# Optimization experiments

Hardware: AMD Instinct MI355X
Metric: run time of the kernel (lower is better)

Reference implementation:

```python
import jax, jax.numpy as jnp
import numpy as np
from jax import lax

EMBED = 512
HEADS = 8
KD = EMBED // HEADS  # key_dim == head_dim (value_factor=1)


def setup_inputs() -> dict:
    key = jax.random.key(0)
    ks = jax.random.split(key, 13)
    b, h, w = 4, 128, 128
    s = 0.02
    return {
        "x": jax.random.normal(ks[0], (b, h, w, EMBED), jnp.float32),
        "mask_h": jax.random.normal(ks[1], (HEADS, h, h), jnp.float32),
        "mask_w": jax.random.normal(ks[2], (HEADS, w, w), jnp.float32),
        "Wq": jax.random.normal(ks[3], (EMBED, EMBED), jnp.float32) * s,
        "bq": jnp.zeros((EMBED,), jnp.float32),
        "Wk": jax.random.normal(ks[4], (EMBED, EMBED), jnp.float32) * s,
        "bk": jnp.zeros((EMBED,), jnp.float32),
        "Wv": jax.random.normal(ks[5], (EMBED, EMBED), jnp.float32) * s,
        "bv": jnp.zeros((EMBED,), jnp.float32),
        "lepe_w": jax.random.normal(ks[6], (5, 5, 1, EMBED), jnp.float32) * s,  # depthwise 5x5, HWIO
        "lepe_b": jnp.zeros((EMBED,), jnp.float32),
        "Wo": jax.random.normal(ks[7], (EMBED, EMBED), jnp.float32) * s,
        "bo": jnp.zeros((EMBED,), jnp.float32),
    }


def reference(x, mask_h, mask_w, Wq, bq, Wk, bk, Wv, bv, lepe_w, lepe_b, Wo, bo):
    b, h, w, _ = x.shape
    scaling = KD ** -0.5
    q = x @ Wq + bq                      # (b,h,w,C)
    k = (x @ Wk + bk) * scaling
    v = x @ Wv + bv

    # depthwise-conv positional term (LePE), 5x5 pad 2, groups=C
    lepe = lax.conv_general_dilated(
        v, lepe_w, window_strides=(1, 1), padding=[(2, 2), (2, 2)],
        dimension_numbers=("NHWC", "HWIO", "NHWC"), feature_group_count=EMBED,
    ) + lepe_b

    qr = q.reshape(b, h, w, HEADS, KD)
    kr = k.reshape(b, h, w, HEADS, KD)
    vr = v.reshape(b, h, w, HEADS, KD)

    # width-axis attention (per row), additive per-head decay mask
    sw = jnp.einsum("bhqnd,bhknd->bhnqk", qr, kr) + mask_w[None, None]  # (b,h,n,w,w)
    Aw = jax.nn.softmax(sw, axis=-1)
    o1 = jnp.einsum("bhnqk,bhknd->bhqnd", Aw, vr)                       # (b,h,w,n,d)

    # height-axis attention (per column) on the width-pass output
    sh = jnp.einsum("bqwnd,bkwnd->bwnqk", qr, kr) + mask_h[None, None]  # (b,w,n,h,h)
    Ah = jax.nn.softmax(sh, axis=-1)
    o2 = jnp.einsum("bwnqk,bkwnd->bqwnd", Ah, o1)                       # (b,h,w,n,d)

    out = o2.reshape(b, h, w, EMBED) + lepe
    return out @ Wo + bo
```

## Files before the change

kernel.cpp:

```cpp
#include <hip/hip_runtime.h>
#include <stdint.h>
#include <stddef.h>

typedef unsigned short u16;
typedef __attribute__((ext_vector_type(8))) short bf16x8;
typedef __attribute__((ext_vector_type(4))) float f32x4;

__device__ __forceinline__ u16 f2bf(float f) {
  union { float f; uint32_t u; } v; v.f = f;
  uint32_t u = v.u;
  return (u16)((u + 0x7FFFu + ((u >> 16) & 1u)) >> 16);
}
__device__ __forceinline__ float bf2f(u16 b) {
  union { uint32_t u; float f; } v; v.u = ((uint32_t)b) << 16;
  return v.f;
}

__device__ __forceinline__ void glds16(const u16* g, u16* l) {
  __builtin_amdgcn_global_load_lds((const __attribute__((address_space(1))) void*)g,
                                   (__attribute__((address_space(3))) void*)l, 16, 0, 0);
}

#define MFMA(a, b, c) __builtin_amdgcn_mfma_f32_16x16x32_bf16((a), (b), (c), 0, 0, 0)


__global__ __launch_bounds__(256) void k_cvt_bf16(const float* __restrict__ in,
                                                  u16* __restrict__ out, int n) {
  int i = (blockIdx.x * 256 + threadIdx.x) * 8;
  if (i >= n) return;
  const float4* p = (const float4*)(in + i);
  float4 a = p[0], b = p[1];
  union { bf16x8 v; u16 s[8]; } o;
  o.s[0] = f2bf(a.x); o.s[1] = f2bf(a.y); o.s[2] = f2bf(a.z); o.s[3] = f2bf(a.w);
  o.s[4] = f2bf(b.x); o.s[5] = f2bf(b.y); o.s[6] = f2bf(b.z); o.s[7] = f2bf(b.w);
  *(bf16x8*)(out + i) = o.v;
}

__global__ __launch_bounds__(256) void k_build_wqkv(
    const float* __restrict__ Wq, const float* __restrict__ bq,
    const float* __restrict__ Wk, const float* __restrict__ bk,
    const float* __restrict__ Wv, const float* __restrict__ bv,
    u16* __restrict__ wT, float* __restrict__ bias) {
  int idx = blockIdx.x * 256 + threadIdx.x;
  int n = idx >> 9, k = idx & 511;
  const float* W; const float* B; int nn; float s = 1.0f;
  if (n < 512)       { W = Wq; B = bq; nn = n; }
  else if (n < 1024) { W = Wk; B = bk; nn = n - 512; s = 0.125f; }
  else               { W = Wv; B = bv; nn = n - 1024; }
  wT[idx] = f2bf(W[(size_t)k * 512 + nn] * s);
  if (k == 0) bias[n] = B[nn] * s;
}

__global__ __launch_bounds__(256) void k_build_wo(const float* __restrict__ Wo,
                                                  u16* __restrict__ wT) {
  int idx = blockIdx.x * 256 + threadIdx.x;
  int n = idx >> 9, k = idx & 511;
  wT[idx] = f2bf(Wo[(size_t)k * 512 + n]);
}


__device__ __forceinline__ void stageH(const u16* __restrict__ src, int ld, size_t grow0,
                                       int kt, int row0, u16* lmat, int t) {
  #pragma unroll
  for (int it = 0; it < 2; ++it) {
    int e = it * 4096 + t * 8;
    int row = row0 + (e >> 6);
    int ch = (e >> 3) & 7;
    int cs = ch ^ (row & 7);
    glds16(src + (grow0 + row) * (size_t)ld + kt * 64 + cs * 8, lmat + row * 64 + ch * 8);
  }
}

__device__ __forceinline__ bf16x8 ldfrag(const u16* lmat, int row, int c) {
  return *(const bf16x8*)(lmat + row * 64 + ((c ^ (row & 7)) << 3));
}

template<bool STAGE, bool VM8>
__device__ __forceinline__ void process_tile(
    const u16* __restrict__ A, int lda, size_t rowA0,
    const u16* __restrict__ BT, int ldb, size_t rowB0,
    u16* LAc, u16* LBc, int nxt,
    int wm, int wn, int fq, int fr, int t,
    f32x4 (&acc)[2][4][2][2])
{
  bf16x8 bA[4][2], bB[2][2][2];
  #pragma unroll
  for (int n = 0; n < 2; ++n)
    #pragma unroll
    for (int kk = 0; kk < 2; ++kk)
      bB[0][n][kk] = ldfrag(LBc, wn * 32 + n * 16 + fr, kk * 4 + fq);
  #pragma unroll
  for (int m = 0; m < 4; ++m)
    #pragma unroll
    for (int kk = 0; kk < 2; ++kk)
      bA[m][kk] = ldfrag(LAc, wm * 64 + m * 16 + fr, kk * 4 + fq);
  __builtin_amdgcn_s_setprio(1);
  #pragma unroll
  for (int m = 0; m < 4; ++m)
    #pragma unroll
    for (int n = 0; n < 2; ++n)
      #pragma unroll
      for (int kk = 0; kk < 2; ++kk)
        acc[0][m][0][n] = MFMA(bA[m][kk], bB[0][n][kk], acc[0][m][0][n]);
  __builtin_amdgcn_s_setprio(0);
  __builtin_amdgcn_s_barrier();
  #pragma unroll
  for (int n = 0; n < 2; ++n)
    #pragma unroll
    for (int kk = 0; kk < 2; ++kk)
      bB[1][n][kk] = ldfrag(LBc, 128 + wn * 32 + n * 16 + fr, kk * 4 + fq);
  if (STAGE) {
    stageH(A, lda, rowA0, nxt, 0, LAc, t);
    stageH(BT, ldb, rowB0, nxt, 0, LBc, t);
  }
  __builtin_amdgcn_s_setprio(1);
  #pragma unroll
  for (int m = 0; m < 4; ++m)
    #pragma unroll
    for (int n = 0; n < 2; ++n)
      #pragma unroll
      for (int kk = 0; kk < 2; ++kk)
        acc[0][m][1][n] = MFMA(bA[m][kk], bB[1][n][kk], acc[0][m][1][n]);
  __builtin_amdgcn_s_setprio(0);
  __builtin_amdgcn_s_barrier();
  #pragma unroll
  for (int m = 0; m < 4; ++m)
    #pragma unroll
    for (int kk = 0; kk < 2; ++kk)
      bA[m][kk] = ldfrag(LAc, 128 + wm * 64 + m * 16 + fr, kk * 4 + fq);
  if (STAGE) stageH(BT, ldb, rowB0, nxt, 128, LBc, t);
  __builtin_amdgcn_s_setprio(1);
  #pragma unroll
  for (int m = 0; m < 4; ++m)
    #pragma unroll
    for (int n = 0; n < 2; ++n)
      #pragma unroll
      for (int kk = 0; kk < 2; ++kk)
        acc[1][m][0][n] = MFMA(bA[m][kk], bB[0][n][kk], acc[1][m][0][n]);
  __builtin_amdgcn_s_setprio(0);
  __builtin_amdgcn_s_barrier();
  if (STAGE) stageH(A, lda, rowA0, nxt, 128, LAc, t);
  __builtin_amdgcn_s_setprio(1);
  #pragma unroll
  for (int m = 0; m < 4; ++m)
    #pragma unroll
    for (int n = 0; n < 2; ++n)
      #pragma unroll
      for (int kk = 0; kk < 2; ++kk)
        acc[1][m][1][n] = MFMA(bA[m][kk], bB[1][n][kk], acc[1][m][1][n]);
  __builtin_amdgcn_s_setprio(0);
  if (VM8) asm volatile("s_waitcnt vmcnt(8)" ::: "memory");
  else     asm volatile("s_waitcnt vmcnt(0)" ::: "memory");
  __builtin_amdgcn_s_barrier();
}

template<bool OUT_F32, int NTN>
__global__ __launch_bounds__(512, 2) void k_gemm256(
    const u16* __restrict__ A, int lda,
    const u16* __restrict__ BT, int ldb,
    const float* __restrict__ bias,
    void* __restrict__ Cp, int ldc)
{
  __shared__ u16 lds[65536];
  u16* LA0 = lds;
  u16* LB0 = lds + 16384;
  u16* LA1 = lds + 32768;
  u16* LB1 = lds + 49152;

  const int t = threadIdx.x, l = t & 63, w = t >> 6;
  const int wm = w >> 2, wn = w & 3;
  const int fq = l >> 4, fr = l & 15;

  const int bid = blockIdx.x;
  const int cpx = gridDim.x >> 3;
  const int swz = (bid & 7) * cpx + (bid >> 3);
  const int tn = swz % NTN, tm = swz / NTN;
  const size_t rowA0 = (size_t)tm * 256;
  const size_t rowB0 = (size_t)tn * 256;

  f32x4 acc[2][4][2][2];
  #pragma unroll
  for (int a = 0; a < 2; ++a)
    #pragma unroll
    for (int m = 0; m < 4; ++m)
      #pragma unroll
      for (int b = 0; b < 2; ++b)
        #pragma unroll
        for (int n = 0; n < 2; ++n) acc[a][m][b][n] = (f32x4){0.f, 0.f, 0.f, 0.f};

  stageH(A,  lda, rowA0, 0, 0,   LA0, t); stageH(A,  lda, rowA0, 0, 128, LA0, t);
  stageH(BT, ldb, rowB0, 0, 0,   LB0, t); stageH(BT, ldb, rowB0, 0, 128, LB0, t);
  stageH(A,  lda, rowA0, 1, 0,   LA1, t); stageH(A,  lda, rowA0, 1, 128, LA1, t);
  stageH(BT, ldb, rowB0, 1, 0,   LB1, t); stageH(BT, ldb, rowB0, 1, 128, LB1, t);
  asm volatile("s_waitcnt vmcnt(8)" ::: "memory");
  __builtin_amdgcn_s_barrier();

  for (int i = 0; i < 3; ++i) {
    process_tile<true, true>(A, lda, rowA0, BT, ldb, rowB0, LA0, LB0, 2 * i + 2,
                             wm, wn, fq, fr, t, acc);
    process_tile<true, true>(A, lda, rowA0, BT, ldb, rowB0, LA1, LB1, 2 * i + 3,
                             wm, wn, fq, fr, t, acc);
  }
  process_tile<false, false>(A, lda, rowA0, BT, ldb, rowB0, LA0, LB0, 0,
                             wm, wn, fq, fr, t, acc);
  process_tile<false, false>(A, lda, rowA0, BT, ldb, rowB0, LA1, LB1, 0,
                             wm, wn, fq, fr, t, acc);

  #pragma unroll
  for (int nh = 0; nh < 2; ++nh)
    #pragma unroll
    for (int n = 0; n < 2; ++n) {
      int col = (int)rowB0 + nh * 128 + wn * 32 + n * 16 + fr;
      float bb = bias[col];
      #pragma unroll
      for (int mh = 0; mh < 2; ++mh)
        #pragma unroll
        for (int m = 0; m < 4; ++m) {
          #pragma unroll
          for (int r = 0; r < 4; ++r) {
            size_t row = rowA0 + mh * 128 + wm * 64 + m * 16 + fq * 4 + r;
            float v = acc[mh][m][nh][n][r] + bb;
            if (OUT_F32) ((float*)Cp)[row * ldc + col] = v;
            else         ((u16*)Cp)[row * ldc + col] = f2bf(v);
          }
        }
    }
}


__global__ __launch_bounds__(256) void k_lepe(
    const u16* __restrict__ qkv, const float* __restrict__ w5,
    const float* __restrict__ lb, u16* __restrict__ outp)
{
  __shared__ u16 wlds[12800];
  #pragma unroll
  for (int j = 0; j < 50; ++j) {
    int idx = j * 256 + threadIdx.x;
    wlds[idx] = f2bf(w5[idx]);
  }
  __syncthreads();

  const int t = threadIdx.x, w = t >> 6, l = t & 63;
  const int c0 = l << 3;
  const int bid = blockIdx.x;
  const int x = (bid & 31) * 4 + w;
  const int y0 = ((bid >> 5) & 15) * 8;
  const int b = bid >> 9;

  float acc[8][8];
  {
    float4 b0 = *(const float4*)(lb + c0);
    float4 b1 = *(const float4*)(lb + c0 + 4);
    #pragma unroll
    for (int tt = 0; tt < 8; ++tt) {
      acc[tt][0] = b0.x; acc[tt][1] = b0.y; acc[tt][2] = b0.z; acc[tt][3] = b0.w;
      acc[tt][4] = b1.x; acc[tt][5] = b1.y; acc[tt][6] = b1.z; acc[tt][7] = b1.w;
    }
  }

  #pragma unroll
  for (int r = 0; r < 12; ++r) {
    int yy = y0 + r - 2;
    if ((unsigned)yy < 128u) {
      #pragma unroll
      for (int dx = 0; dx < 5; ++dx) {
        int xx = x + dx - 2;
        if ((unsigned)xx < 128u) {
          union { bf16x8 v; u16 s[8]; } v8;
          v8.v = *(const bf16x8*)(qkv + (size_t)((b * 128 + yy) * 128 + xx) * 1536
                                  + 1024 + c0);
          float vf[8];
          #pragma unroll
          for (int j = 0; j < 8; ++j) vf[j] = bf2f(v8.s[j]);
          #pragma unroll
          for (int tt = 0; tt < 8; ++tt) {
            int dy = r - tt;
            if (dy >= 0 && dy <= 4) {
              union { bf16x8 v; u16 s[8]; } w8;
              w8.v = *(const bf16x8*)(wlds + (dy * 5 + dx) * 512 + c0);
              #pragma unroll
              for (int j = 0; j < 8; ++j)
                acc[tt][j] += vf[j] * bf2f(w8.s[j]);
            }
          }
        }
      }
    }
  }

  #pragma unroll
  for (int tt = 0; tt < 8; ++tt) {
    size_t tok = (size_t)(b * 128 + y0 + tt) * 128 + x;
    union { bf16x8 v; u16 s[8]; } ov;
    #pragma unroll
    for (int j = 0; j < 8; ++j) ov.s[j] = f2bf(acc[tt][j]);
    *(bf16x8*)(outp + tok * 512 + c0) = ov.v;
  }
}


template<int AXIS>
__global__ __launch_bounds__(512) void k_attn(
    const u16* qkv, const float* __restrict__ mask,
    const u16* __restrict__ lepe, u16* outp)
{
  __shared__ u16 smem[24576];
  u16* q_s = smem;
  u16* k_s = smem + 8192;
  u16* vT  = smem + 16384;
  u16* P   = smem;

  const int t = threadIdx.x, w = t >> 6, l = t & 63;
  const int fq = l >> 4, fr = l & 15;
  const int line = blockIdx.x, head = blockIdx.y, b = blockIdx.z;
  const int coff = head * 64;
  const size_t base0 = (AXIS == 0) ? ((size_t)(b * 128 + line) * 128)
                                   : ((size_t)b * 16384 + line);
  const size_t tstr = (AXIS == 0) ? 1 : 128;

  #pragma unroll
  for (int it = 0; it < 2; ++it) {
    int ee = it * 4096 + t * 8;
    int row = ee >> 6;
    int cs = ((ee >> 3) & 7) ^ (row & 7);
    size_t tok = base0 + (size_t)row * tstr;
    glds16(qkv + tok * 1536 +       coff + cs * 8, q_s + it * 4096 + w * 512);
    glds16(qkv + tok * 1536 + 512 + coff + cs * 8, k_s + it * 4096 + w * 512);
  }
  {
    int chunk = t & 7, kgrp = t >> 3;
    #pragma unroll
    for (int p = 0; p < 2; ++p) {
      int kidx = p * 64 + kgrp;
      size_t tok = base0 + (size_t)kidx * tstr;
      union { bf16x8 v; u16 s[8]; } v8;
      v8.v = *(const bf16x8*)(qkv + tok * 1536 + 1024 + coff + chunk * 8);
      #pragma unroll
      for (int j = 0; j < 8; ++j) {
        int d = chunk * 8 + j;
        int byt = d * 256 + ((2 * kidx) ^ (j << 4) ^ (chunk << 5));
        *(u16*)((char*)vT + byt) = v8.s[j];
      }
    }
  }
  __syncthreads();

  f32x4 acc[8];
  #pragma unroll
  for (int n = 0; n < 8; ++n) acc[n] = (f32x4){0.f, 0.f, 0.f, 0.f};

  #pragma unroll
  for (int kk = 0; kk < 2; ++kk) {
    int arow = w * 16 + fr;
    int ac = (kk * 4 + fq) ^ (arow & 7);
    bf16x8 af = *(const bf16x8*)(q_s + arow * 64 + ac * 8);
    #pragma unroll
    for (int n = 0; n < 8; ++n) {
      int brow = n * 16 + fr;
      int bc = (kk * 4 + fq) ^ (brow & 7);
      bf16x8 bfr = *(const bf16x8*)(k_s + brow * 64 + bc * 8);
      acc[n] = MFMA(af, bfr, acc[n]);
    }
  }

  const float* mbase = mask + (size_t)head * 16384;
  const int q0 = w * 16 + fq * 4;
  #pragma unroll
  for (int n = 0; n < 8; ++n) {
    const float* mp = mbase + (size_t)q0 * 128 + n * 16 + fr;
    #pragma unroll
    for (int r = 0; r < 4; ++r) acc[n][r] += mp[(size_t)r * 128];
  }
  #pragma unroll
  for (int r = 0; r < 4; ++r) {
    float mx = acc[0][r];
    #pragma unroll
    for (int n = 1; n < 8; ++n) mx = fmaxf(mx, acc[n][r]);
    mx = fmaxf(mx, __shfl_xor(mx, 1));
    mx = fmaxf(mx, __shfl_xor(mx, 2));
    mx = fmaxf(mx, __shfl_xor(mx, 4));
    mx = fmaxf(mx, __shfl_xor(mx, 8));
    float sum = 0.f;
    #pragma unroll
    for (int n = 0; n < 8; ++n) {
      float ev = __expf(acc[n][r] - mx);
      acc[n][r] = ev; sum += ev;
    }
    sum += __shfl_xor(sum, 1);
    sum += __shfl_xor(sum, 2);
    sum += __shfl_xor(sum, 4);
    sum += __shfl_xor(sum, 8);
    float inv = 1.0f / sum;
    #pragma unroll
    for (int n = 0; n < 8; ++n) acc[n][r] *= inv;
  }
  __syncthreads();

  #pragma unroll
  for (int r = 0; r < 4; ++r) {
    int row = q0 + r;
    int swz = (row & 7) << 4;
    #pragma unroll
    for (int n = 0; n < 8; ++n) {
      int col = n * 16 + fr;
      *(u16*)((char*)P + row * 256 + ((2 * col) ^ swz)) = f2bf(acc[n][r]);
    }
  }
  __syncthreads();

  f32x4 o[4];
  #pragma unroll
  for (int n = 0; n < 4; ++n) o[n] = (f32x4){0.f, 0.f, 0.f, 0.f};

  #pragma unroll
  for (int kt = 0; kt < 4; ++kt) {
    int arow = w * 16 + fr;
    bf16x8 af = *(const bf16x8*)((const char*)P + arow * 256 +
                 (((kt * 4 + fq) << 4) ^ ((arow & 7) << 4)));
    #pragma unroll
    for (int n = 0; n < 4; ++n) {
      int d = n * 16 + fr;
      int byt = d * 256 + (((kt * 32 + fq * 8) * 2) ^ ((d & 7) << 4)
                           ^ (((d >> 3) & 7) << 5));
      bf16x8 bfr = *(const bf16x8*)((const char*)vT + byt);
      o[n] = MFMA(af, bfr, o[n]);
    }
  }

  #pragma unroll
  for (int r = 0; r < 4; ++r) {
    int i = q0 + r;
    size_t tok = base0 + (size_t)i * tstr;
    #pragma unroll
    for (int n = 0; n < 4; ++n) {
      int d = n * 16 + fr;
      float v = o[n][r];
      if (AXIS == 1) {
        v += bf2f(lepe[tok * 512 + coff + d]);
        outp[tok * 1536 + coff + d] = f2bf(v);
      } else {
        outp[tok * 1536 + 1024 + coff + d] = f2bf(v);
      }
    }
  }
}


extern "C" void kernel_launch(void* const* d_in, const int* in_sizes, int n_in,
                              void* d_out, int out_size, void* d_ws, size_t ws_size,
                              hipStream_t stream) {
  const float* x  = (const float*)d_in[0];
  const float* mh = (const float*)d_in[1];
  const float* mw = (const float*)d_in[2];
  const float* Wq = (const float*)d_in[3];
  const float* bq = (const float*)d_in[4];
  const float* Wk = (const float*)d_in[5];
  const float* bk = (const float*)d_in[6];
  const float* Wv = (const float*)d_in[7];
  const float* bv = (const float*)d_in[8];
  const float* w5 = (const float*)d_in[9];
  const float* lb = (const float*)d_in[10];
  const float* Wo = (const float*)d_in[11];
  const float* bo = (const float*)d_in[12];

  char* ws = (char*)d_ws;
  u16*   qkv   = (u16*)ws;
  u16*   wqkvT = (u16*)(ws + 201326592);
  u16*   woT   = (u16*)(ws + 202899456);
  float* bqkv  = (float*)(ws + 203423744);

  char* od = (char*)d_out;
  u16* xb   = (u16*)od;
  u16* lepe = (u16*)(od + 67108864);

  k_cvt_bf16<<<16384, 256, 0, stream>>>(x, xb, 33554432);
  k_build_wqkv<<<3072, 256, 0, stream>>>(Wq, bq, Wk, bk, Wv, bv, wqkvT, bqkv);
  k_build_wo<<<1024, 256, 0, stream>>>(Wo, woT);

  k_gemm256<false, 6><<<1536, 512, 0, stream>>>(xb, 512, wqkvT, 512, bqkv, qkv, 1536);

  k_lepe<<<2048, 256, 0, stream>>>(qkv, w5, lb, lepe);

  k_attn<0><<<dim3(128, 8, 4), 512, 0, stream>>>(qkv, mw, nullptr, qkv);
  k_attn<1><<<dim3(128, 8, 4), 512, 0, stream>>>(qkv, mh, lepe, qkv);

  k_gemm256<true, 2><<<512, 512, 0, stream>>>(qkv, 1536, woT, 512, bo, d_out, 512);
}
```

Before: 437.2 us.

## Replace in-place quarter-staged GEMM pipeline with simple double-buffered prefetch

Restructures the 256x256 GEMM main loop. Each tile now issues the full next-k-tile load into the other LDS buffer at the start, then does all fragment loads and MFMAs with a single wait and barrier at the end. Previously each buffer was refilled in place in quarters, with four barriers per tile and two tiles kept in flight. This removes the intra-tile barriers, but the prefetch is only one tile deep and each tile ends with a full vmcnt(0) wait, which may expose more load latency. It also holds more fragment registers at once.

```diff
diff --git a/kernel.cpp b/kernel.cpp
--- a/kernel.cpp
+++ b/kernel.cpp
@@ -75,82 +75,61 @@
   return *(const bf16x8*)(lmat + row * 64 + ((c ^ (row & 7)) << 3));
 }
 
-template<bool STAGE, bool VM8>
-__device__ __forceinline__ void process_tile(
+template<bool PREF>
+__device__ __forceinline__ void ptile(
     const u16* __restrict__ A, int lda, size_t rowA0,
     const u16* __restrict__ BT, int ldb, size_t rowB0,
-    u16* LAc, u16* LBc, int nxt,
+    u16* LAc, u16* LBc, u16* LAo, u16* LBo, int nxt,
     int wm, int wn, int fq, int fr, int t,
     f32x4 (&acc)[2][4][2][2])
 {
-  bf16x8 bA[4][2], bB[2][2][2];
-  #pragma unroll
-  for (int n = 0; n < 2; ++n)
+  if (PREF) {
+    stageH(A,  lda, rowA0, nxt, 0,   LAo, t);
+    stageH(A,  lda, rowA0, nxt, 128, LAo, t);
+    stageH(BT, ldb, rowB0, nxt, 0,   LBo, t);
+    stageH(BT, ldb, rowB0, nxt, 128, LBo, t);
+  }
+  bf16x8 fB[2][2][2], fA[4][2];
+  #pragma unroll
+  for (int nh = 0; nh < 2; ++nh)
+    #pragma unroll
+    for (int n = 0; n < 2; ++n)
+      #pragma unroll
+      for (int kk = 0; kk < 2; ++kk)
+        fB[nh][n][kk] = ldfrag(LBc, nh * 128 + wn * 32 + n * 16 + fr, kk * 4 + fq);
+  #pragma unroll
+  for (int m = 0; m < 4; ++m)
     #pragma unroll
     for (int kk = 0; kk < 2; ++kk)
-      bB[0][n][kk] = ldfrag(LBc, wn * 32 + n * 16 + fr, kk * 4 + fq);
+      fA[m][kk] = ldfrag(LAc, wm * 64 + m * 16 + fr, kk * 4 + fq);
+  __builtin_amdgcn_s_setprio(1);
   #pragma unroll
   for (int m = 0; m < 4; ++m)
     #pragma unroll
+    for (int nh = 0; nh < 2; ++nh)
+      #pragma unroll
+      for (int n = 0; n < 2; ++n)
+        #pragma unroll
+        for (int kk = 0; kk < 2; ++kk)
+          acc[0][m][nh][n] = MFMA(fA[m][kk], fB[nh][n][kk], acc[0][m][nh][n]);
+  __builtin_amdgcn_s_setprio(0);
+  #pragma unroll
+  for (int m = 0; m < 4; ++m)
+    #pragma unroll
     for (int kk = 0; kk < 2; ++kk)
-      bA[m][kk] = ldfrag(LAc, wm * 64 + m * 16 + fr, kk * 4 + fq);
+      fA[m][kk] = ldfrag(LAc, 128 + wm * 64 + m * 16 + fr, kk * 4 + fq);
   __builtin_amdgcn_s_setprio(1);
   #pragma unroll
   for (int m = 0; m < 4; ++m)
     #pragma unroll
-    for (int n = 0; n < 2; ++n)
-      #pragma unroll
-      for (int kk = 0; kk < 2; ++kk)
-        acc[0][m][0][n] = MFMA(bA[m][kk], bB[0][n][kk], acc[0][m][0][n]);
+    for (int nh = 0; nh < 2; ++nh)
+      #pragma unroll
+      for (int n = 0; n < 2; ++n)
+        #pragma unroll
+        for (int kk = 0; kk < 2; ++kk)
+          acc[1][m][nh][n] = MFMA(fA[m][kk], fB[nh][n][kk], acc[1][m][nh][n]);
   __builtin_amdgcn_s_setprio(0);
-  __builtin_amdgcn_s_barrier();
-  #pragma unroll
-  for (int n = 0; n < 2; ++n)
-    #pragma unroll
-    for (int kk = 0; kk < 2; ++kk)
-      bB[1][n][kk] = ldfrag(LBc, 128 + wn * 32 + n * 16 + fr, kk * 4 + fq);
-  if (STAGE) {
-    stageH(A, lda, rowA0, nxt, 0, LAc, t);
-    stageH(BT, ldb, rowB0, nxt, 0, LBc, t);
-  }
-  __builtin_amdgcn_s_setprio(1);
-  #pragma unroll
-  for (int m = 0; m < 4; ++m)
-    #pragma unroll
-    for (int n = 0; n < 2; ++n)
-      #pragma unroll
-      for (int kk = 0; kk < 2; ++kk)
-        acc[0][m][1][n] = MFMA(bA[m][kk], bB[1][n][kk], acc[0][m][1][n]);
-  __builtin_amdgcn_s_setprio(0);
-  __builtin_amdgcn_s_barrier();
-  #pragma unroll
-  for (int m = 0; m < 4; ++m)
-    #pragma unroll
-    for (int kk = 0; kk < 2; ++kk)
-      bA[m][kk] = ldfrag(LAc, 128 + wm * 64 + m * 16 + fr, kk * 4 + fq);
-  if (STAGE) stageH(BT, ldb, rowB0, nxt, 128, LBc, t);
-  __builtin_amdgcn_s_setprio(1);
-  #pragma unroll
-  for (int m = 0; m < 4; ++m)
-    #pragma unroll
-    for (int n = 0; n < 2; ++n)
-      #pragma unroll
-      for (int kk = 0; kk < 2; ++kk)
-        acc[1][m][0][n] = MFMA(bA[m][kk], bB[0][n][kk], acc[1][m][0][n]);
-  __builtin_amdgcn_s_setprio(0);
-  __builtin_amdgcn_s_barrier();
-  if (STAGE) stageH(A, lda, rowA0, nxt, 128, LAc, t);
-  __builtin_amdgcn_s_setprio(1);
-  #pragma unroll
-  for (int m = 0; m < 4; ++m)
-    #pragma unroll
-    for (int n = 0; n < 2; ++n)
-      #pragma unroll
-      for (int kk = 0; kk < 2; ++kk)
-        acc[1][m][1][n] = MFMA(bA[m][kk], bB[1][n][kk], acc[1][m][1][n]);
-  __builtin_amdgcn_s_setprio(0);
-  if (VM8) asm volatile("s_waitcnt vmcnt(8)" ::: "memory");
-  else     asm volatile("s_waitcnt vmcnt(0)" ::: "memory");
+  asm volatile("s_waitcnt vmcnt(0)" ::: "memory");
   __builtin_amdgcn_s_barrier();
 }
 
@@ -190,21 +169,19 @@
 
   stageH(A,  lda, rowA0, 0, 0,   LA0, t); stageH(A,  lda, rowA0, 0, 128, LA0, t);
   stageH(BT, ldb, rowB0, 0, 0,   LB0, t); stageH(BT, ldb, rowB0, 0, 128, LB0, t);
-  stageH(A,  lda, rowA0, 1, 0,   LA1, t); stageH(A,  lda, rowA0, 1, 128, LA1, t);
-  stageH(BT, ldb, rowB0, 1, 0,   LB1, t); stageH(BT, ldb, rowB0, 1, 128, LB1, t);
-  asm volatile("s_waitcnt vmcnt(8)" ::: "memory");
+  asm volatile("s_waitcnt vmcnt(0)" ::: "memory");
   __builtin_amdgcn_s_barrier();
 
   for (int i = 0; i < 3; ++i) {
-    process_tile<true, true>(A, lda, rowA0, BT, ldb, rowB0, LA0, LB0, 2 * i + 2,
-                             wm, wn, fq, fr, t, acc);
-    process_tile<true, true>(A, lda, rowA0, BT, ldb, rowB0, LA1, LB1, 2 * i + 3,
-                             wm, wn, fq, fr, t, acc);
-  }
-  process_tile<false, false>(A, lda, rowA0, BT, ldb, rowB0, LA0, LB0, 0,
-                             wm, wn, fq, fr, t, acc);
-  process_tile<false, false>(A, lda, rowA0, BT, ldb, rowB0, LA1, LB1, 0,
-                             wm, wn, fq, fr, t, acc);
+    ptile<true>(A, lda, rowA0, BT, ldb, rowB0, LA0, LB0, LA1, LB1, 2 * i + 1,
+                wm, wn, fq, fr, t, acc);
+    ptile<true>(A, lda, rowA0, BT, ldb, rowB0, LA1, LB1, LA0, LB0, 2 * i + 2,
+                wm, wn, fq, fr, t, acc);
+  }
+  ptile<true>(A, lda, rowA0, BT, ldb, rowB0, LA0, LB0, LA1, LB1, 7,
+              wm, wn, fq, fr, t, acc);
+  ptile<false>(A, lda, rowA0, BT, ldb, rowB0, LA1, LB1, LA0, LB0, 0,
+               wm, wn, fq, fr, t, acc);
 
   #pragma unroll
   for (int nh = 0; nh < 2; ++nh)
```

Measured after the change: 485.5 us. 11.0% more time.

## Stage bf16 GEMM epilogue through LDS and merge weight-transpose kernels

Applied to the files above, without the earlier changes.

The bf16-output GEMM epilogue now writes biased results into a swizzled LDS tile and then emits 16-byte row-contiguous global stores, replacing scattered 2-byte stores. The two weight-transpose kernels are merged into one tiled LDS transpose kernel with coalesced reads and writes, which also cuts a launch. The epilogue adds two barriers per half-tile and relies on the existing LDS buffer being large enough for 128x256 bf16.

```diff
diff --git a/kernel.cpp b/kernel.cpp
--- a/kernel.cpp
+++ b/kernel.cpp
@@ -36,26 +36,42 @@
   *(bf16x8*)(out + i) = o.v;
 }
 
-__global__ __launch_bounds__(256) void k_build_wqkv(
-    const float* __restrict__ Wq, const float* __restrict__ bq,
-    const float* __restrict__ Wk, const float* __restrict__ bk,
-    const float* __restrict__ Wv, const float* __restrict__ bv,
-    u16* __restrict__ wT, float* __restrict__ bias) {
-  int idx = blockIdx.x * 256 + threadIdx.x;
-  int n = idx >> 9, k = idx & 511;
-  const float* W; const float* B; int nn; float s = 1.0f;
-  if (n < 512)       { W = Wq; B = bq; nn = n; }
-  else if (n < 1024) { W = Wk; B = bk; nn = n - 512; s = 0.125f; }
-  else               { W = Wv; B = bv; nn = n - 1024; }
-  wT[idx] = f2bf(W[(size_t)k * 512 + nn] * s);
-  if (k == 0) bias[n] = B[nn] * s;
-}
-
-__global__ __launch_bounds__(256) void k_build_wo(const float* __restrict__ Wo,
-                                                  u16* __restrict__ wT) {
-  int idx = blockIdx.x * 256 + threadIdx.x;
-  int n = idx >> 9, k = idx & 511;
-  wT[idx] = f2bf(Wo[(size_t)k * 512 + n]);
+
+__global__ __launch_bounds__(256) void k_build_w(
+    const float* __restrict__ Wq, const float* __restrict__ Wk,
+    const float* __restrict__ Wv, const float* __restrict__ Wo,
+    const float* __restrict__ bq, const float* __restrict__ bk,
+    const float* __restrict__ bv,
+    u16* __restrict__ wqkvT, u16* __restrict__ woT, float* __restrict__ bias)
+{
+  __shared__ u16 tl[64 * 73];
+  const int bid = blockIdx.x;
+  const int mtx = bid >> 6;
+  const int tr = (bid >> 3) & 7, tc = bid & 7;
+  const float* W = (mtx == 0) ? Wq : (mtx == 1) ? Wk : (mtx == 2) ? Wv : Wo;
+  const float s = (mtx == 1) ? 0.125f : 1.0f;
+  const int t = threadIdx.x;
+  const int lr = t >> 6, lc = t & 63;
+  #pragma unroll
+  for (int it = 0; it < 16; ++it) {
+    int k = tr * 64 + it * 4 + lr;
+    int n = tc * 64 + lc;
+    tl[lc * 73 + it * 4 + lr] = f2bf(W[(size_t)k * 512 + n] * s);
+  }
+  __syncthreads();
+  u16* dst = (mtx == 3) ? woT : (wqkvT + (size_t)mtx * 512 * 512);
+  #pragma unroll
+  for (int it = 0; it < 16; ++it) {
+    int n = tc * 64 + it * 4 + lr;
+    int k = tr * 64 + lc;
+    dst[(size_t)n * 512 + k] = tl[(it * 4 + lr) * 73 + lc];
+  }
+  if (bid < 6) {
+    int i = bid * 256 + t;
+    const float* B = (i < 512) ? bq : (i < 1024) ? bk : bv;
+    float sc = (i >= 512 && i < 1024) ? 0.125f : 1.0f;
+    bias[i] = B[i & 511] * sc;
+  }
 }
 
 
@@ -206,25 +222,55 @@
   process_tile<false, false>(A, lda, rowA0, BT, ldb, rowB0, LA1, LB1, 0,
                              wm, wn, fq, fr, t, acc);
 
-  #pragma unroll
-  for (int nh = 0; nh < 2; ++nh)
-    #pragma unroll
-    for (int n = 0; n < 2; ++n) {
-      int col = (int)rowB0 + nh * 128 + wn * 32 + n * 16 + fr;
-      float bb = bias[col];
-      #pragma unroll
-      for (int mh = 0; mh < 2; ++mh)
+  if (OUT_F32) {
+    #pragma unroll
+    for (int nh = 0; nh < 2; ++nh)
+      #pragma unroll
+      for (int n = 0; n < 2; ++n) {
+        int col = (int)rowB0 + nh * 128 + wn * 32 + n * 16 + fr;
+        float bb = bias[col];
         #pragma unroll
-        for (int m = 0; m < 4; ++m) {
+        for (int mh = 0; mh < 2; ++mh)
           #pragma unroll
-          for (int r = 0; r < 4; ++r) {
-            size_t row = rowA0 + mh * 128 + wm * 64 + m * 16 + fq * 4 + r;
-            float v = acc[mh][m][nh][n][r] + bb;
-            if (OUT_F32) ((float*)Cp)[row * ldc + col] = v;
-            else         ((u16*)Cp)[row * ldc + col] = f2bf(v);
-          }
+          for (int m = 0; m < 4; ++m)
+            #pragma unroll
+            for (int r = 0; r < 4; ++r) {
+              size_t row = rowA0 + mh * 128 + wm * 64 + m * 16 + fq * 4 + r;
+              ((float*)Cp)[row * ldc + col] = acc[mh][m][nh][n][r] + bb;
+            }
+      }
+  } else {
+    #pragma unroll
+    for (int mh = 0; mh < 2; ++mh) {
+      #pragma unroll
+      for (int nh = 0; nh < 2; ++nh)
+        #pragma unroll
+        for (int n = 0; n < 2; ++n) {
+          int col = nh * 128 + wn * 32 + n * 16 + fr;
+          float bb = bias[(int)rowB0 + col];
+          #pragma unroll
+          for (int m = 0; m < 4; ++m)
+            #pragma unroll
+            for (int r = 0; r < 4; ++r) {
+              int row = wm * 64 + m * 16 + fq * 4 + r;
+              int ch = (col >> 3) ^ (row & 7);
+              lds[row * 256 + ch * 8 + (col & 7)] = f2bf(acc[mh][m][nh][n][r] + bb);
+            }
         }
-    }
+      __syncthreads();
+      {
+        int row = t >> 2, q = t & 3;
+        #pragma unroll
+        for (int j = 0; j < 8; ++j) {
+          int ch = (q * 8 + j) ^ (row & 7);
+          bf16x8 v = *(const bf16x8*)(lds + row * 256 + ch * 8);
+          *(bf16x8*)((u16*)Cp + (rowA0 + mh * 128 + row) * (size_t)ldc
+                     + rowB0 + q * 64 + j * 8) = v;
+        }
+      }
+      __syncthreads();
+    }
+  }
 }
 
 
@@ -474,8 +520,7 @@
   u16* lepe = (u16*)(od + 67108864);
 
   k_cvt_bf16<<<16384, 256, 0, stream>>>(x, xb, 33554432);
-  k_build_wqkv<<<3072, 256, 0, stream>>>(Wq, bq, Wk, bk, Wv, bv, wqkvT, bqkv);
-  k_build_wo<<<1024, 256, 0, stream>>>(Wo, woT);
+  k_build_w<<<256, 256, 0, stream>>>(Wq, Wk, Wv, Wo, bq, bk, bv, wqkvT, woT, bqkv);
 
   k_gemm256<false, 6><<<1536, 512, 0, stream>>>(xb, 512, wqkvT, 512, bqkv, qkv, 1536);
 
```

Result: slower. 465.8 us (+6.5%).
